# Kernel optimization log

Hardware: AMD Instinct MI355X
Metric: run time of the kernel (lower is better)

The kernel has to match this reference:

```python
import jax, jax.numpy as jnp
import numpy as np

ALPHA = 4.0   # spikingjelly sigmoid surrogate alpha
TAU = 2.0
EPS = 1e-5
NUM_HEADS = 8

@jax.custom_vjp
def spike(x):
    return (x >= 0.0).astype(x.dtype)

def _spike_fwd(x):
    return spike(x), x

def _spike_bwd(x, g):
    s = jax.nn.sigmoid(ALPHA * x)
    return (g * ALPHA * s * (1.0 - s),)

spike.defvjp(_spike_fwd, _spike_bwd)

def lif(x):
    # Multi-step LIF over leading time axis T; hard reset to 0, detach_reset=True.
    def step(v, xt):
        h = v + (xt - v) / TAU
        s = spike(h - 1.0)
        v_new = (1.0 - jax.lax.stop_gradient(s)) * h
        return v_new, s
    _, out = jax.lax.scan(step, jnp.zeros_like(x[0]), x)
    return out

def bn(x, gamma, beta):
    # x: (T*B, N, D). torch applies BatchNorm1d on (T*B, D, N): per-channel-D
    # batch stats over (T*B, N) dims (training mode, biased var).
    mean = x.mean(axis=(0, 1))
    var = x.var(axis=(0, 1))
    return (x - mean) * jax.lax.rsqrt(var + EPS) * gamma + beta

def proximity_mask(T):
    # assumed create_temporal_proximity_mask: weight decays with |i-j|
    idx = jnp.arange(T)
    return 1.0 / (1.0 + jnp.abs(idx[:, None] - idx[None, :]).astype(jnp.float32))

def _branch(x, W, g, b, T, B, H, d):
    D = H * d
    y = bn(x.reshape(T * B, -1, D) @ W.T, g, b)
    return lif(y.reshape(T, B, -1, H, d))  # (T,B,N,H,d)

def _forward(q, kv, Wq, gq, bq, Wk, gk, bk, Wv, gv, bv, Wp, gp, bp):
    T, B, N, D = q.shape
    H = NUM_HEADS
    d = D // H
    scale = D ** (-0.5)
    mask = proximity_mask(T)  # (T,T)

    qh = _branch(q, Wq, gq, bq, T, B, H, d)   # (T,B,N,H,d)
    kh = _branch(kv, Wk, gk, bk, T, B, H, d)  # (T,B,N,H,d)
    vh = _branch(kv, Wv, gv, bv, T, B, H, d)  # (T,B,N,H,d)

    # torch: k,v transposed over (time, token) axes before matmul.
    # scores[x,b,h,i,j] = sum_d q[x,b,i,h,d] * k[j,b,x,h,d]
    scores = jnp.einsum('xbihd,jbxhd->xbhij', qh, kh)
    scores = scores * mask[None, None, None, :, :]
    # z[x,b,h,i,d] = sum_j scores[x,b,h,i,j] * v[j,b,x,h,d]
    z = jnp.einsum('xbhij,jbxhd->xbhid', scores, vh) * scale

    # permute(3,1,0,2,4) -> (i=N, B, x=T, H, d); reshape to (T,B,T,D)
    z = z.transpose(3, 1, 0, 2, 4).reshape(T, B, T, D)
    z = lif(z)  # attn_lif

    y = z.reshape(T * B, T, D) @ Wp.T
    y = bn(y, gp, bp).reshape(T, B, T, D)
    y = lif(y)  # proj_lif; dropout is identity (eval)
    return y

def setup_inputs() -> dict:
    T, B, N, D = 64, 8, 64, 384
    key = jax.random.key(0)
    ks = jax.random.split(key, 6)
    w = lambda k: (jax.random.normal(k, (D, D), dtype=jnp.float32) * 0.02)
    return {
        'q': jax.random.normal(ks[0], (T, B, N, D), dtype=jnp.float32),
        'kv': jax.random.normal(ks[1], (T, B, N, D), dtype=jnp.float32),
        'Wq': w(ks[2]), 'gq': jnp.ones((D,), jnp.float32), 'bq': jnp.zeros((D,), jnp.float32),
        'Wk': w(ks[3]), 'gk': jnp.ones((D,), jnp.float32), 'bk': jnp.zeros((D,), jnp.float32),
        'Wv': w(ks[4]), 'gv': jnp.ones((D,), jnp.float32), 'bv': jnp.zeros((D,), jnp.float32),
        'Wp': w(ks[5]), 'gp': jnp.ones((D,), jnp.float32), 'bp': jnp.zeros((D,), jnp.float32),
    }

def reference(q, kv, Wq, gq, bq, Wk, gk, bk, Wv, gv, bv, Wp, gp, bp):
    return _forward(q, kv, Wq, gq, bq, Wk, gk, bk, Wv, gv, bv, Wp, gp, bp)
```

## Files before the change

kernel.cpp:

```cpp
#include <hip/hip_runtime.h>

typedef unsigned char u8;
typedef unsigned short u16;
typedef unsigned int u32;
typedef unsigned long long u64;
typedef __attribute__((ext_vector_type(8))) short s16x8;
typedef __attribute__((ext_vector_type(4))) float f32x4;

#define T_DIM 64
#define B_DIM 8
#define N_DIM 64
#define D_DIM 384
#define H_DIM 8
#define HD 48
#define M_ROWS 32768
#define CH 196608
#define STATS_BLOCKS 256

#define IMG_PER_KSTEP 16384
#define IMG_PER_NTILE (12 * IMG_PER_KSTEP)
#define IMG_PER_W (3 * IMG_PER_NTILE)

__device__ __forceinline__ void split8(const float* e, int4& o1, int4& o2, int4& o3) {
  u16 h1[8], h2[8], h3[8];
#pragma unroll
  for (int i = 0; i < 8; ++i) {
    const float x = e[i];
    const u32 b = __float_as_uint(x);
    h1[i] = (u16)(b >> 16);
    const float x1 = __uint_as_float(b & 0xFFFF0000u);
    const float r1 = x - x1;
    const u32 c = __float_as_uint(r1);
    h2[i] = (u16)(c >> 16);
    const float x2 = __uint_as_float(c & 0xFFFF0000u);
    const float r2 = r1 - x2;
    h3[i] = (u16)(__float_as_uint(r2) >> 16);
  }
  o1 = make_int4((int)((u32)h1[0] | ((u32)h1[1] << 16)), (int)((u32)h1[2] | ((u32)h1[3] << 16)),
                 (int)((u32)h1[4] | ((u32)h1[5] << 16)), (int)((u32)h1[6] | ((u32)h1[7] << 16)));
  o2 = make_int4((int)((u32)h2[0] | ((u32)h2[1] << 16)), (int)((u32)h2[2] | ((u32)h2[3] << 16)),
                 (int)((u32)h2[4] | ((u32)h2[5] << 16)), (int)((u32)h2[6] | ((u32)h2[7] << 16)));
  o3 = make_int4((int)((u32)h3[0] | ((u32)h3[1] << 16)), (int)((u32)h3[2] | ((u32)h3[3] << 16)),
                 (int)((u32)h3[4] | ((u32)h3[5] << 16)), (int)((u32)h3[6] | ((u32)h3[7] << 16)));
}

__device__ __forceinline__ void split8_2(const float* e, int4& o1, int4& o2) {
  u16 h1[8], h2[8];
#pragma unroll
  for (int i = 0; i < 8; ++i) {
    const float x = e[i];
    const u32 b = __float_as_uint(x);
    h1[i] = (u16)(b >> 16);
    const float x1 = __uint_as_float(b & 0xFFFF0000u);
    const float r1 = x - x1;
    h2[i] = (u16)(__float_as_uint(r1) >> 16);
  }
  o1 = make_int4((int)((u32)h1[0] | ((u32)h1[1] << 16)), (int)((u32)h1[2] | ((u32)h1[3] << 16)),
                 (int)((u32)h1[4] | ((u32)h1[5] << 16)), (int)((u32)h1[6] | ((u32)h1[7] << 16)));
  o2 = make_int4((int)((u32)h2[0] | ((u32)h2[1] << 16)), (int)((u32)h2[2] | ((u32)h2[3] << 16)),
                 (int)((u32)h2[4] | ((u32)h2[5] << 16)), (int)((u32)h2[6] | ((u32)h2[7] << 16)));
}

__device__ __forceinline__ void split1(float xx, u16& a, u16& b2, u16& c) {
  const u32 u = __float_as_uint(xx);
  a = (u16)(u >> 16);
  const float x1 = __uint_as_float(u & 0xFFFF0000u);
  const float r1 = xx - x1;
  const u32 u2 = __float_as_uint(r1);
  b2 = (u16)(u2 >> 16);
  const float x2 = __uint_as_float(u2 & 0xFFFF0000u);
  const float r2 = r1 - x2;
  c = (u16)(__float_as_uint(r2) >> 16);
}

__device__ __forceinline__ u64 packmask48(const u8* p) {
  const int4 r0 = ((const int4*)p)[0];
  const int4 r1 = ((const int4*)p)[1];
  const int4 r2 = ((const int4*)p)[2];
  u32 wv[12] = {(u32)r0.x, (u32)r0.y, (u32)r0.z, (u32)r0.w,
                (u32)r1.x, (u32)r1.y, (u32)r1.z, (u32)r1.w,
                (u32)r2.x, (u32)r2.y, (u32)r2.z, (u32)r2.w};
  u64 bits = 0;
#pragma unroll
  for (int w = 0; w < 12; ++w) {
    const u32 u = wv[w];
    const u32 nib = (u & 1u) | ((u >> 7) & 2u) | ((u >> 14) & 4u) | ((u >> 21) & 8u);
    bits |= (u64)nib << (w * 4);
  }
  return bits;
}

__global__ __launch_bounds__(256) void prep_w(const float* __restrict__ W0,
                                              const float* __restrict__ W1,
                                              const float* __restrict__ W2,
                                              const float* __restrict__ W3,
                                              char* __restrict__ img) {
  const int widx = blockIdx.x & 3;
  const int nt = blockIdx.x >> 2;
  const float* W = (widx == 0) ? W0 : (widx == 1) ? W1 : (widx == 2) ? W2 : W3;
  char* base = img + (size_t)widx * IMG_PER_W + (size_t)nt * IMG_PER_NTILE;
  const int tid = threadIdx.x;
  const int nr = tid >> 1;
  const int kh = tid & 1;
  for (int ks = 0; ks < 12; ++ks) {
    const float* src = W + (size_t)(nt * 128 + nr) * D_DIM + ks * 32 + kh * 16;
    float4 v0 = ((const float4*)src)[0];
    float4 v1 = ((const float4*)src)[1];
    float4 v2 = ((const float4*)src)[2];
    float4 v3 = ((const float4*)src)[3];
    float e[16] = {v0.x, v0.y, v0.z, v0.w, v1.x, v1.y, v1.z, v1.w,
                   v2.x, v2.y, v2.z, v2.w, v3.x, v3.y, v3.z, v3.w};
    int4* dst = (int4*)(base + (size_t)ks * IMG_PER_KSTEP);
#pragma unroll
    for (int sub = 0; sub < 2; ++sub) {
      const int kc = kh * 2 + sub;
      int4 o1, o2, o3;
      split8(e + sub * 8, o1, o2, o3);
      dst[(0 * 4 + kc) * 128 + (nr ^ kc)] = o1;
      dst[(1 * 4 + kc) * 128 + (nr ^ kc)] = o2;
    }
  }
}

template <int ASPL>
__global__ __launch_bounds__(256) void gemm_bn(const void* __restrict__ Ain,
                                               const char* __restrict__ imgW,
                                               float* __restrict__ C,
                                               double* __restrict__ part) {
  constexpr int ABYTES = ASPL * 8192;
  __shared__ __align__(16) char shraw[ABYTES + 16384];
  int4* AchW = (int4*)shraw;
  int4* BchW = (int4*)(shraw + ABYTES);
  const s16x8* AchR = (const s16x8*)shraw;
  const s16x8* BchR = (const s16x8*)(shraw + ABYTES);

  const int tid = threadIdx.x;
  const int lane = tid & 63;
  const int w = tid >> 6;
  const int wm = w >> 1, wn = w & 1;
  const int lr = lane & 15;
  const int kcL = lane >> 4;
  const int bn = blockIdx.x * 128;
  const int by = blockIdx.y;
  const int bm = by * 128;

  const int4* imgI = (const int4*)(imgW + (size_t)blockIdx.x * IMG_PER_NTILE);

  int axc[4], bxc[4];
#pragma unroll
  for (int f = 0; f < 4; ++f) {
    axc[f] = kcL * 128 + ((wm * 64 + f * 16 + lr) ^ kcL);
    bxc[f] = kcL * 128 + ((wn * 64 + f * 16 + lr) ^ kcL);
  }

  float4 a0, a1, a2, a3;
  int4 za0, za1;
  int4 b0, b1, b2, b3;

  const int arow = tid >> 1, akh = tid & 1;
  const int c0 = tid, c1 = tid + 256;

#define LOADA(ks)                                                             \
  do {                                                                        \
    if (ASPL == 2) {                                                          \
      const float* ap = (const float*)Ain + (size_t)(bm + arow) * D_DIM +     \
                        (ks) * 32 + akh * 16;                                 \
      a0 = ((const float4*)ap)[0]; a1 = ((const float4*)ap)[1];               \
      a2 = ((const float4*)ap)[2]; a3 = ((const float4*)ap)[3];               \
    } else {                                                                  \
      const u16* zp = (const u16*)Ain;                                        \
      { const int kc = c0 >> 7, mp = c0 & 127;                                \
        za0 = *(const int4*)(zp + (size_t)(bm + (mp ^ kc)) * D_DIM +          \
                             (ks) * 32 + kc * 8); }                           \
      { const int kc = c1 >> 7, mp = c1 & 127;                                \
        za1 = *(const int4*)(zp + (size_t)(bm + (mp ^ kc)) * D_DIM +          \
                             (ks) * 32 + kc * 8); }                           \
    }                                                                         \
  } while (0)

#define LOADB(ks)                                                             \
  do {                                                                        \
    b0 = imgI[(ks) * 1024 + tid];                                             \
    b1 = imgI[(ks) * 1024 + tid + 256];                                       \
    b2 = imgI[(ks) * 1024 + tid + 512];                                       \
    b3 = imgI[(ks) * 1024 + tid + 768];                                       \
  } while (0)

#define WRITES()                                                              \
  do {                                                                        \
    if (ASPL == 2) {                                                          \
      float e0[8] = {a0.x, a0.y, a0.z, a0.w, a1.x, a1.y, a1.z, a1.w};         \
      float e1[8] = {a2.x, a2.y, a2.z, a2.w, a3.x, a3.y, a3.z, a3.w};         \
      int4 o1, o2;                                                            \
      { const int kc = akh * 2;                                               \
        split8_2(e0, o1, o2);                                                 \
        AchW[0 * 512 + kc * 128 + (arow ^ kc)] = o1;                          \
        AchW[1 * 512 + kc * 128 + (arow ^ kc)] = o2; }                        \
      { const int kc = akh * 2 + 1;                                           \
        split8_2(e1, o1, o2);                                                 \
        AchW[0 * 512 + kc * 128 + (arow ^ kc)] = o1;                          \
        AchW[1 * 512 + kc * 128 + (arow ^ kc)] = o2; }                        \
    } else {                                                                  \
      AchW[c0] = za0; AchW[c1] = za1;                                         \
    }                                                                         \
    BchW[tid] = b0; BchW[tid + 256] = b1;                                     \
    BchW[tid + 512] = b2; BchW[tid + 768] = b3;                               \
  } while (0)

  f32x4 acc[4][4] = {};

  LOADA(0); LOADB(0);
  WRITES();
  __syncthreads();

  for (int ks = 0; ks < 12; ++ks) {
    if (ks < 11) { LOADA(ks + 1); LOADB(ks + 1); }
    s16x8 af[ASPL][4];
#pragma unroll
    for (int s = 0; s < ASPL; ++s)
#pragma unroll
      for (int fm = 0; fm < 4; ++fm) af[s][fm] = AchR[s * 512 + axc[fm]];
#pragma unroll
    for (int fn = 0; fn < 4; ++fn) {
      const s16x8 bf0 = BchR[bxc[fn]];
      const s16x8 bf1 = BchR[512 + bxc[fn]];
      if (ASPL == 2) {
#pragma unroll
        for (int fm = 0; fm < 4; ++fm)
          acc[fm][fn] = __builtin_amdgcn_mfma_f32_16x16x32_bf16(af[ASPL - 1][fm], bf0, acc[fm][fn], 0, 0, 0);
      }
#pragma unroll
      for (int fm = 0; fm < 4; ++fm)
        acc[fm][fn] = __builtin_amdgcn_mfma_f32_16x16x32_bf16(af[0][fm], bf1, acc[fm][fn], 0, 0, 0);
#pragma unroll
      for (int fm = 0; fm < 4; ++fm)
        acc[fm][fn] = __builtin_amdgcn_mfma_f32_16x16x32_bf16(af[0][fm], bf0, acc[fm][fn], 0, 0, 0);
    }
    __syncthreads();
    if (ks < 11) { WRITES(); __syncthreads(); }
  }
#undef LOADA
#undef LOADB
#undef WRITES

#pragma unroll
  for (int fm = 0; fm < 4; ++fm)
#pragma unroll
    for (int fn = 0; fn < 4; ++fn) {
      const int row = bm + wm * 64 + fm * 16 + kcL * 4;
      const int col = bn + wn * 64 + fn * 16 + lr;
#pragma unroll
      for (int r = 0; r < 4; ++r)
        C[(size_t)(row + r) * D_DIM + col] = acc[fm][fn][r];
    }

  double* red = (double*)shraw;
#pragma unroll
  for (int fn = 0; fn < 4; ++fn) {
    const int col = wn * 64 + fn * 16 + lr;
    const int rg = wm * 4 + kcL;
    double s = 0.0, qd = 0.0;
#pragma unroll
    for (int fm = 0; fm < 4; ++fm)
#pragma unroll
      for (int r = 0; r < 4; ++r) {
        const double v = (double)acc[fm][fn][r];
        s += v;
        qd += v * v;
      }
    red[(rg * 128 + col) * 2 + 0] = s;
    red[(rg * 128 + col) * 2 + 1] = qd;
  }
  __syncthreads();
  if (tid < 128) {
    double S = 0.0, Q = 0.0;
#pragma unroll
    for (int rg = 0; rg < 8; ++rg) {
      S += red[(rg * 128 + tid) * 2 + 0];
      Q += red[(rg * 128 + tid) * 2 + 1];
    }
    const size_t pidx = ((size_t)by * D_DIM + bn + tid) * 2;
    part[pidx + 0] = S;
    part[pidx + 1] = Q;
  }
}

__global__ void bn_stats_final(const double* __restrict__ part,
                               const float* __restrict__ gamma,
                               const float* __restrict__ beta,
                               float* __restrict__ ss) {
  const int c = blockIdx.x * 64 + threadIdx.x;
  double s = 0.0, q = 0.0;
  for (int b = 0; b < STATS_BLOCKS; ++b) {
    s += part[((size_t)b * D_DIM + c) * 2 + 0];
    q += part[((size_t)b * D_DIM + c) * 2 + 1];
  }
  const double n = (double)M_ROWS;
  const double mean = s / n;
  const double var = q / n - mean * mean;
  const double rstd = 1.0 / sqrt(var + 1e-5);
  const double sc = (double)gamma[c] * rstd;
  ss[c * 2 + 0] = (float)sc;
  ss[c * 2 + 1] = (float)((double)beta[c] - mean * sc);
}

template <int MODE>
__global__ __launch_bounds__(256) void lif_kernel(float* Y,
                                                  const float* __restrict__ ss,
                                                  u8* __restrict__ spikes) {
  const int c = blockIdx.x * 256 + threadIdx.x;
  const int dd = c % D_DIM;
  const float scale = ss[dd * 2 + 0];
  const float shift = ss[dd * 2 + 1];
  float v = 0.0f;
  for (int t0 = 0; t0 < T_DIM; t0 += 8) {
    float xs[8];
#pragma unroll
    for (int u = 0; u < 8; ++u) xs[u] = Y[(size_t)(t0 + u) * CH + c];
#pragma unroll
    for (int u = 0; u < 8; ++u) {
      const float xv = xs[u] * scale + shift;
      const float hh = v + (xv - v) * 0.5f;
      const float sp = (hh >= 1.0f) ? 1.0f : 0.0f;
      v = (1.0f - sp) * hh;
      if (MODE == 0)
        spikes[(size_t)(t0 + u) * CH + c] = (u8)sp;
      else
        Y[(size_t)(t0 + u) * CH + c] = sp;
    }
  }
}

__global__ __launch_bounds__(64) void attn_kernel(const u8* __restrict__ qs,
                                                  const u8* __restrict__ ks,
                                                  const u8* __restrict__ vs,
                                                  u16* __restrict__ z) {
  const int gid = blockIdx.x;
  const int h = gid & 7;
  const int b = (gid >> 3) & 7;
  const int x = gid >> 6;
  const int lane = threadIdx.x;

  __shared__ union {
    struct { u64 qm[64]; u64 km[64]; float maskT[64]; u16 vt[48][80]; } a;
    struct { float zl[64][50]; } zz;
  } sh;

  {
    const u8* qp = qs + ((size_t)((x * B_DIM + b) * N_DIM + lane)) * D_DIM + h * HD;
    sh.a.qm[lane] = packmask48(qp);
    const size_t koff = ((size_t)((lane * B_DIM + b) * N_DIM + x)) * D_DIM + h * HD;
    sh.a.km[lane] = packmask48(ks + koff);
    const u8* vp = vs + koff;
    const int4 r0 = ((const int4*)vp)[0];
    const int4 r1 = ((const int4*)vp)[1];
    const int4 r2 = ((const int4*)vp)[2];
    u32 vw[12] = {(u32)r0.x, (u32)r0.y, (u32)r0.z, (u32)r0.w,
                  (u32)r1.x, (u32)r1.y, (u32)r1.z, (u32)r1.w,
                  (u32)r2.x, (u32)r2.y, (u32)r2.z, (u32)r2.w};
#pragma unroll
    for (int w = 0; w < 12; ++w) {
      const u32 u = vw[w];
#pragma unroll
      for (int e = 0; e < 4; ++e)
        sh.a.vt[w * 4 + e][lane] = ((u >> (8 * e)) & 1u) ? (u16)0x3F80 : (u16)0;
    }
    sh.a.maskT[lane] = 1.0f / (float)(1 + lane);
  }
  __syncthreads();

  const int lr = lane & 15;
  const int lg = lane >> 4;
  f32x4 acc[4][3] = {};

  for (int ksi = 0; ksi < 2; ++ksi) {
    const int j0 = lg * 8 + ksi * 32;
    s16x8 bf[3];
#pragma unroll
    for (int nf = 0; nf < 3; ++nf)
      bf[nf] = *(const s16x8*)&sh.a.vt[lr + nf * 16][j0];
    s16x8 af[3][4];
#pragma unroll
    for (int mf = 0; mf < 4; ++mf) {
      const int i = lr + mf * 16;
      const u64 qi = sh.a.qm[i];
      union { u32 w[4]; s16x8 v; } p1, p2, p3;
#pragma unroll
      for (int pp = 0; pp < 4; ++pp) {
        u16 aa[2], bb[2], cc[2];
#pragma unroll
        for (int e = 0; e < 2; ++e) {
          const int j = j0 + pp * 2 + e;
          const int cnt = __popcll(qi & sh.a.km[j]);
          int ad = i - j;
          if (ad < 0) ad = -ad;
          const float sv = (float)cnt * sh.a.maskT[ad];
          split1(sv, aa[e], bb[e], cc[e]);
        }
        p1.w[pp] = (u32)aa[0] | ((u32)aa[1] << 16);
        p2.w[pp] = (u32)bb[0] | ((u32)bb[1] << 16);
        p3.w[pp] = (u32)cc[0] | ((u32)cc[1] << 16);
      }
      af[0][mf] = p1.v;
      af[1][mf] = p2.v;
      af[2][mf] = p3.v;
    }
#pragma unroll
    for (int spi = 0; spi < 3; ++spi) {
      const int sp = 2 - spi;
#pragma unroll
      for (int nf = 0; nf < 3; ++nf)
#pragma unroll
        for (int mf = 0; mf < 4; ++mf)
          acc[mf][nf] = __builtin_amdgcn_mfma_f32_16x16x32_bf16(af[sp][mf], bf[nf],
                                                                acc[mf][nf], 0, 0, 0);
    }
  }
  __syncthreads();

  const float kScale = 0.05103103630798287f;
#pragma unroll
  for (int mf = 0; mf < 4; ++mf)
#pragma unroll
    for (int nf = 0; nf < 3; ++nf)
#pragma unroll
      for (int r = 0; r < 4; ++r)
        sh.zz.zl[mf * 16 + lg * 4 + r][lr + nf * 16] = acc[mf][nf][r] * kScale;
  __syncthreads();

  if (lane < HD) {
    float v = 0.0f;
    for (int i0 = 0; i0 < 64; i0 += 8) {
      float zv[8];
#pragma unroll
      for (int u = 0; u < 8; ++u) zv[u] = sh.zz.zl[i0 + u][lane];
#pragma unroll
      for (int u = 0; u < 8; ++u) {
        const float hh = v + (zv[u] - v) * 0.5f;
        const u16 sp16 = (hh >= 1.0f) ? (u16)0x3F80 : (u16)0;
        v = (hh >= 1.0f) ? 0.0f : hh;
        z[((size_t)(((i0 + u) * B_DIM + b) * T_DIM + x)) * D_DIM + h * HD + lane] = sp16;
      }
    }
  }
}

extern "C" void kernel_launch(void* const* d_in, const int* in_sizes, int n_in,
                              void* d_out, int out_size, void* d_ws, size_t ws_size,
                              hipStream_t stream) {
  const float* q  = (const float*)d_in[0];
  const float* kv = (const float*)d_in[1];
  const float* Wq = (const float*)d_in[2];
  const float* gq = (const float*)d_in[3];
  const float* bq = (const float*)d_in[4];
  const float* Wk = (const float*)d_in[5];
  const float* gk = (const float*)d_in[6];
  const float* bk = (const float*)d_in[7];
  const float* Wv = (const float*)d_in[8];
  const float* gv = (const float*)d_in[9];
  const float* bv = (const float*)d_in[10];
  const float* Wp = (const float*)d_in[11];
  const float* gp = (const float*)d_in[12];
  const float* bp = (const float*)d_in[13];
  float* out = (float*)d_out;
  char* ws = (char*)d_ws;

  float* Ybuf  = (float*)(ws + 0);
  u16*   Zb    = (u16*)(ws + 0);
  double* part = (double*)(ws + 50331648ull);
  float* ss    = (float*)(ws + 51904512ull);
  u8* qsb      = (u8*)(ws + 51907584ull);
  u8* ksb      = (u8*)(ws + 64490496ull);
  u8* vsb      = (u8*)(ws + 77073408ull);
  char* Wimg   = (char*)(ws + 89656320ull);

  dim3 gg(3, 256);

  prep_w<<<12, 256, 0, stream>>>(Wq, Wk, Wv, Wp, Wimg);

  gemm_bn<2><<<gg, 256, 0, stream>>>(q, Wimg + 0 * (size_t)IMG_PER_W, Ybuf, part);
  bn_stats_final<<<6, 64, 0, stream>>>(part, gq, bq, ss);
  lif_kernel<0><<<CH / 256, 256, 0, stream>>>(Ybuf, ss, qsb);

  gemm_bn<2><<<gg, 256, 0, stream>>>(kv, Wimg + 1 * (size_t)IMG_PER_W, Ybuf, part);
  bn_stats_final<<<6, 64, 0, stream>>>(part, gk, bk, ss);
  lif_kernel<0><<<CH / 256, 256, 0, stream>>>(Ybuf, ss, ksb);

  gemm_bn<2><<<gg, 256, 0, stream>>>(kv, Wimg + 2 * (size_t)IMG_PER_W, Ybuf, part);
  bn_stats_final<<<6, 64, 0, stream>>>(part, gv, bv, ss);
  lif_kernel<0><<<CH / 256, 256, 0, stream>>>(Ybuf, ss, vsb);

  attn_kernel<<<T_DIM * B_DIM * H_DIM, 64, 0, stream>>>(qsb, ksb, vsb, Zb);

  gemm_bn<1><<<gg, 256, 0, stream>>>(Zb, Wimg + 3 * (size_t)IMG_PER_W, out, part);
  bn_stats_final<<<6, 64, 0, stream>>>(part, gp, bp, ss);
  lif_kernel<2><<<CH / 256, 256, 0, stream>>>(out, ss, (u8*)nullptr);
}
```

Measured before the change: 281.2 us.

## Double-buffer GEMM A-tile registers and pack four heads per attention block

The GEMM main loop is unrolled by two with two register sets for the A tile, so the global loads for step k+2 are issued while step k computes. This lengthens the prefetch distance to hide load latency, at the cost of higher register pressure. Separately, the attention kernel now runs four heads per 256-thread block, each wave with its own shared-memory slab. This gives fewer, larger blocks with more shared memory per block.

```diff
diff --git a/kernel.cpp b/kernel.cpp
--- a/kernel.cpp
+++ b/kernel.cpp
@@ -153,28 +153,28 @@
     bxc[f] = kcL * 128 + ((wn * 64 + f * 16 + lr) ^ kcL);
   }
 
-  float4 a0, a1, a2, a3;
-  int4 za0, za1;
+  float4 a00, a01, a02, a03, a10, a11, a12, a13;
+  int4 z00, z01, z10, z11;
   int4 b0, b1, b2, b3;
 
   const int arow = tid >> 1, akh = tid & 1;
   const int c0 = tid, c1 = tid + 256;
 
-#define LOADA(ks)                                                             \
+#define LOADA_(ks, r0, r1, r2, r3, q0, q1)                                    \
   do {                                                                        \
     if (ASPL == 2) {                                                          \
       const float* ap = (const float*)Ain + (size_t)(bm + arow) * D_DIM +     \
                         (ks) * 32 + akh * 16;                                 \
-      a0 = ((const float4*)ap)[0]; a1 = ((const float4*)ap)[1];               \
-      a2 = ((const float4*)ap)[2]; a3 = ((const float4*)ap)[3];               \
+      r0 = ((const float4*)ap)[0]; r1 = ((const float4*)ap)[1];               \
+      r2 = ((const float4*)ap)[2]; r3 = ((const float4*)ap)[3];               \
     } else {                                                                  \
       const u16* zp = (const u16*)Ain;                                        \
       { const int kc = c0 >> 7, mp = c0 & 127;                                \
-        za0 = *(const int4*)(zp + (size_t)(bm + (mp ^ kc)) * D_DIM +          \
-                             (ks) * 32 + kc * 8); }                           \
+        q0 = *(const int4*)(zp + (size_t)(bm + (mp ^ kc)) * D_DIM +           \
+                            (ks) * 32 + kc * 8); }                            \
       { const int kc = c1 >> 7, mp = c1 & 127;                                \
-        za1 = *(const int4*)(zp + (size_t)(bm + (mp ^ kc)) * D_DIM +          \
-                             (ks) * 32 + kc * 8); }                           \
+        q1 = *(const int4*)(zp + (size_t)(bm + (mp ^ kc)) * D_DIM +           \
+                            (ks) * 32 + kc * 8); }                            \
     }                                                                         \
   } while (0)
 
@@ -186,11 +186,11 @@
     b3 = imgI[(ks) * 1024 + tid + 768];                                       \
   } while (0)
 
-#define WRITES()                                                              \
+#define WRITEA_(r0, r1, r2, r3, q0, q1)                                       \
   do {                                                                        \
     if (ASPL == 2) {                                                          \
-      float e0[8] = {a0.x, a0.y, a0.z, a0.w, a1.x, a1.y, a1.z, a1.w};         \
-      float e1[8] = {a2.x, a2.y, a2.z, a2.w, a3.x, a3.y, a3.z, a3.w};         \
+      float e0[8] = {r0.x, r0.y, r0.z, r0.w, r1.x, r1.y, r1.z, r1.w};         \
+      float e1[8] = {r2.x, r2.y, r2.z, r2.w, r3.x, r3.y, r3.z, r3.w};         \
       int4 o1, o2;                                                            \
       { const int kc = akh * 2;                                               \
         split8_2(e0, o1, o2);                                                 \
@@ -201,47 +201,76 @@
         AchW[0 * 512 + kc * 128 + (arow ^ kc)] = o1;                          \
         AchW[1 * 512 + kc * 128 + (arow ^ kc)] = o2; }                        \
     } else {                                                                  \
-      AchW[c0] = za0; AchW[c1] = za1;                                         \
+      AchW[c0] = q0; AchW[c1] = q1;                                           \
     }                                                                         \
+  } while (0)
+
+#define WRITEB()                                                              \
+  do {                                                                        \
     BchW[tid] = b0; BchW[tid + 256] = b1;                                     \
     BchW[tid + 512] = b2; BchW[tid + 768] = b3;                               \
   } while (0)
 
+#define COMPUTE()                                                             \
+  do {                                                                        \
+    s16x8 af[ASPL][4];                                                        \
+    _Pragma("unroll")                                                         \
+    for (int s = 0; s < ASPL; ++s)                                            \
+      _Pragma("unroll")                                                       \
+      for (int fm = 0; fm < 4; ++fm) af[s][fm] = AchR[s * 512 + axc[fm]];     \
+    _Pragma("unroll")                                                         \
+    for (int fn = 0; fn < 4; ++fn) {                                          \
+      const s16x8 bf0 = BchR[bxc[fn]];                                        \
+      const s16x8 bf1 = BchR[512 + bxc[fn]];                                  \
+      if (ASPL == 2) {                                                        \
+        _Pragma("unroll")                                                     \
+        for (int fm = 0; fm < 4; ++fm)                                        \
+          acc[fm][fn] = __builtin_amdgcn_mfma_f32_16x16x32_bf16(              \
+              af[ASPL - 1][fm], bf0, acc[fm][fn], 0, 0, 0);                   \
+      }                                                                       \
+      _Pragma("unroll")                                                       \
+      for (int fm = 0; fm < 4; ++fm)                                          \
+        acc[fm][fn] = __builtin_amdgcn_mfma_f32_16x16x32_bf16(                \
+            af[0][fm], bf1, acc[fm][fn], 0, 0, 0);                            \
+      _Pragma("unroll")                                                       \
+      for (int fm = 0; fm < 4; ++fm)                                          \
+        acc[fm][fn] = __builtin_amdgcn_mfma_f32_16x16x32_bf16(                \
+            af[0][fm], bf0, acc[fm][fn], 0, 0, 0);                            \
+    }                                                                         \
+  } while (0)
+
   f32x4 acc[4][4] = {};
 
-  LOADA(0); LOADB(0);
-  WRITES();
+  LOADA_(0, a00, a01, a02, a03, z00, z01);
+  LOADB(0);
+  WRITEA_(a00, a01, a02, a03, z00, z01);
+  WRITEB();
   __syncthreads();
-
-  for (int ks = 0; ks < 12; ++ks) {
-    if (ks < 11) { LOADA(ks + 1); LOADB(ks + 1); }
-    s16x8 af[ASPL][4];
-#pragma unroll
-    for (int s = 0; s < ASPL; ++s)
-#pragma unroll
-      for (int fm = 0; fm < 4; ++fm) af[s][fm] = AchR[s * 512 + axc[fm]];
-#pragma unroll
-    for (int fn = 0; fn < 4; ++fn) {
-      const s16x8 bf0 = BchR[bxc[fn]];
-      const s16x8 bf1 = BchR[512 + bxc[fn]];
-      if (ASPL == 2) {
-#pragma unroll
-        for (int fm = 0; fm < 4; ++fm)
-          acc[fm][fn] = __builtin_amdgcn_mfma_f32_16x16x32_bf16(af[ASPL - 1][fm], bf0, acc[fm][fn], 0, 0, 0);
-      }
-#pragma unroll
-      for (int fm = 0; fm < 4; ++fm)
-        acc[fm][fn] = __builtin_amdgcn_mfma_f32_16x16x32_bf16(af[0][fm], bf1, acc[fm][fn], 0, 0, 0);
-#pragma unroll
-      for (int fm = 0; fm < 4; ++fm)
-        acc[fm][fn] = __builtin_amdgcn_mfma_f32_16x16x32_bf16(af[0][fm], bf0, acc[fm][fn], 0, 0, 0);
-    }
+  LOADA_(1, a10, a11, a12, a13, z10, z11);
+
+  for (int ks = 0; ks < 12; ks += 2) {
+    LOADB(ks + 1);
+    if (ks + 2 < 12) LOADA_(ks + 2, a00, a01, a02, a03, z00, z01);
+    COMPUTE();
     __syncthreads();
-    if (ks < 11) { WRITES(); __syncthreads(); }
-  }
-#undef LOADA
+    WRITEA_(a10, a11, a12, a13, z10, z11);
+    WRITEB();
+    __syncthreads();
+    if (ks + 2 < 12) LOADB(ks + 2);
+    if (ks + 3 < 12) LOADA_(ks + 3, a10, a11, a12, a13, z10, z11);
+    COMPUTE();
+    __syncthreads();
+    if (ks + 2 < 12) {
+      WRITEA_(a00, a01, a02, a03, z00, z01);
+      WRITEB();
+      __syncthreads();
+    }
+  }
+#undef LOADA_
 #undef LOADB
-#undef WRITES
+#undef WRITEA_
+#undef WRITEB
+#undef COMPUTE
 
 #pragma unroll
   for (int fm = 0; fm < 4; ++fm)
@@ -331,26 +360,30 @@
   }
 }
 
-__global__ __launch_bounds__(64) void attn_kernel(const u8* __restrict__ qs,
-                                                  const u8* __restrict__ ks,
-                                                  const u8* __restrict__ vs,
-                                                  u16* __restrict__ z) {
+__global__ __launch_bounds__(256) void attn_kernel(const u8* __restrict__ qs,
+                                                   const u8* __restrict__ ks,
+                                                   const u8* __restrict__ vs,
+                                                   u16* __restrict__ z) {
   const int gid = blockIdx.x;
-  const int h = gid & 7;
-  const int b = (gid >> 3) & 7;
-  const int x = gid >> 6;
-  const int lane = threadIdx.x;
-
-  __shared__ union {
+  const int hg = (gid & 1) * 4;
+  const int b = (gid >> 1) & 7;
+  const int x = gid >> 4;
+  const int w = threadIdx.x >> 6;
+  const int h = hg + w;
+  const int lane = threadIdx.x & 63;
+
+  union Slab {
     struct { u64 qm[64]; u64 km[64]; float maskT[64]; u16 vt[48][80]; } a;
-    struct { float zl[64][50]; } zz;
-  } sh;
+    float zl[64][50];
+  };
+  __shared__ Slab sh[4];
+  Slab& S = sh[w];
 
   {
     const u8* qp = qs + ((size_t)((x * B_DIM + b) * N_DIM + lane)) * D_DIM + h * HD;
-    sh.a.qm[lane] = packmask48(qp);
+    S.a.qm[lane] = packmask48(qp);
     const size_t koff = ((size_t)((lane * B_DIM + b) * N_DIM + x)) * D_DIM + h * HD;
-    sh.a.km[lane] = packmask48(ks + koff);
+    S.a.km[lane] = packmask48(ks + koff);
     const u8* vp = vs + koff;
     const int4 r0 = ((const int4*)vp)[0];
     const int4 r1 = ((const int4*)vp)[1];
@@ -359,13 +392,13 @@
                   (u32)r1.x, (u32)r1.y, (u32)r1.z, (u32)r1.w,
                   (u32)r2.x, (u32)r2.y, (u32)r2.z, (u32)r2.w};
 #pragma unroll
-    for (int w = 0; w < 12; ++w) {
-      const u32 u = vw[w];
+    for (int ww = 0; ww < 12; ++ww) {
+      const u32 u = vw[ww];
 #pragma unroll
       for (int e = 0; e < 4; ++e)
-        sh.a.vt[w * 4 + e][lane] = ((u >> (8 * e)) & 1u) ? (u16)0x3F80 : (u16)0;
-    }
-    sh.a.maskT[lane] = 1.0f / (float)(1 + lane);
+        S.a.vt[ww * 4 + e][lane] = ((u >> (8 * e)) & 1u) ? (u16)0x3F80 : (u16)0;
+    }
+    S.a.maskT[lane] = 1.0f / (float)(1 + lane);
   }
   __syncthreads();
 
@@ -378,12 +411,12 @@
     s16x8 bf[3];
 #pragma unroll
     for (int nf = 0; nf < 3; ++nf)
-      bf[nf] = *(const s16x8*)&sh.a.vt[lr + nf * 16][j0];
+      bf[nf] = *(const s16x8*)&S.a.vt[lr + nf * 16][j0];
     s16x8 af[3][4];
 #pragma unroll
     for (int mf = 0; mf < 4; ++mf) {
       const int i = lr + mf * 16;
-      const u64 qi = sh.a.qm[i];
+      const u64 qi = S.a.qm[i];
       union { u32 w[4]; s16x8 v; } p1, p2, p3;
 #pragma unroll
       for (int pp = 0; pp < 4; ++pp) {
@@ -391,10 +424,10 @@
 #pragma unroll
         for (int e = 0; e < 2; ++e) {
           const int j = j0 + pp * 2 + e;
-          const int cnt = __popcll(qi & sh.a.km[j]);
+          const int cnt = __popcll(qi & S.a.km[j]);
           int ad = i - j;
           if (ad < 0) ad = -ad;
-          const float sv = (float)cnt * sh.a.maskT[ad];
+          const float sv = (float)cnt * S.a.maskT[ad];
           split1(sv, aa[e], bb[e], cc[e]);
         }
         p1.w[pp] = (u32)aa[0] | ((u32)aa[1] << 16);
@@ -425,7 +458,7 @@
     for (int nf = 0; nf < 3; ++nf)
 #pragma unroll
       for (int r = 0; r < 4; ++r)
-        sh.zz.zl[mf * 16 + lg * 4 + r][lr + nf * 16] = acc[mf][nf][r] * kScale;
+        S.zl[mf * 16 + lg * 4 + r][lr + nf * 16] = acc[mf][nf][r] * kScale;
   __syncthreads();
 
   if (lane < HD) {
@@ -433,7 +466,7 @@
     for (int i0 = 0; i0 < 64; i0 += 8) {
       float zv[8];
 #pragma unroll
-      for (int u = 0; u < 8; ++u) zv[u] = sh.zz.zl[i0 + u][lane];
+      for (int u = 0; u < 8; ++u) zv[u] = S.zl[i0 + u][lane];
 #pragma unroll
       for (int u = 0; u < 8; ++u) {
         const float hh = v + (zv[u] - v) * 0.5f;
@@ -490,7 +523,7 @@
   bn_stats_final<<<6, 64, 0, stream>>>(part, gv, bv, ss);
   lif_kernel<0><<<CH / 256, 256, 0, stream>>>(Ybuf, ss, vsb);
 
-  attn_kernel<<<T_DIM * B_DIM * H_DIM, 64, 0, stream>>>(qsb, ksb, vsb, Zb);
+  attn_kernel<<<T_DIM * B_DIM * 2, 256, 0, stream>>>(qsb, ksb, vsb, Zb);
 
   gemm_bn<1><<<gg, 256, 0, stream>>>(Zb, Wimg + 3 * (size_t)IMG_PER_W, out, part);
   bn_stats_final<<<6, 64, 0, stream>>>(part, gp, bp, ss);
```

After: 274.4 us. 1.02x faster.
